# Optimization experiments

Measured on AMD Instinct MI355X. Metric: run time of the kernel, lower is better.

Reference implementation:

```python
import jax, jax.numpy as jnp
import numpy as np
from jax import lax

MSIZE = 64
NREG = 9
POOL_W = 256


def conv2d(x, w, b, stride):
    y = lax.conv_general_dilated(x, w, (stride, stride), ((1, 1), (1, 1)),
                                 dimension_numbers=('NCHW', 'OIHW', 'NCHW'))
    return y + b[None, :, None, None]


def resize_nearest(m, h, w):
    # nearest-neighbor resize of a 2D integer mask (matches cv2 INTER_NEAREST floor mapping)
    H, W = m.shape
    ri = (np.arange(h) * H) // h
    ci = (np.arange(w) * W) // w
    return m[ri][:, ci]


def adaptive_max_1d(x, out_size):
    # x: (c, N) -> (c, out_size), torch AdaptiveMaxPool semantics along last dim
    N = x.shape[1]
    j = np.arange(out_size)
    starts = (j * N) // out_size
    ends = -((-(j + 1) * N) // out_size)  # ceil((j+1)*N/out)
    maxlen = int((ends - starts).max())
    idx = starts[:, None] + np.arange(maxlen)[None, :]  # (out, maxlen)
    valid = idx < ends[:, None]
    idx = np.minimum(idx, N - 1)
    g = x[:, idx]  # (c, out, maxlen)
    g = jnp.where(valid[None, :, :], g, -jnp.inf)
    return g.max(axis=2)


def image_cnn(x, masks_np, w1, b1, w2, b2, w3, b3, fcw, fcb):
    f = jax.nn.relu(conv2d(x, w1, b1, 2))
    f = jax.nn.relu(conv2d(f, w2, b2, 2))
    f = conv2d(f, w3, b3, 2)
    _, c, h, w = f.shape
    ff = f.reshape(c, h * w)
    mats = {}
    for i in range(NREG):
        m = resize_nearest(masks_np[i, 0], h, w).reshape(-1)
        if int((m == 1).sum()) >= 10:
            idx = np.nonzero(m == 1)[0]
            pooled = adaptive_max_1d(ff[:, idx], POOL_W)  # (16, 256)
            mats[i] = fcw @ pooled.reshape(-1) + fcb      # (MSIZE*MSIZE,)
    return mats


def mul_forward(cF, sF, content, style, cmasks_np, smasks_np,
                compress_w, compress_b, unzip_w, unzip_b, sp, cp):
    sb, sc, sh, sw = sF.shape
    X = jnp.einsum('oc,bchw->bohw', compress_w, cF) + compress_b[None, :, None, None]
    cb, cc, ch, cw = X.shape
    X = X.reshape(cc, ch * cw)
    X = X - X.mean(axis=1, keepdims=True)
    sM = image_cnn(style, smasks_np, *sp)
    cM = image_cnn(content, cmasks_np, *cp)
    sFF = sF.reshape(sc, sh * sw)
    trans = X
    fmean = jnp.zeros((sc, ch * cw), dtype=cF.dtype)
    for i in range(NREG):
        cm = resize_nearest(cmasks_np[i, 0], ch, cw).reshape(-1)
        sm = resize_nearest(smasks_np[i, 0], sh, sw).reshape(-1)
        if int((cm == 1).sum()) >= 10 and int((sm == 1).sum()) >= 10 and i in sM and i in cM:
            fgc = np.nonzero(cm == 1)[0]
            fgs = np.nonzero(sm == 1)[0]
            sMean = sFF[:, fgs].mean(axis=1, keepdims=True)            # (sc, 1)
            T = sM[i].reshape(MSIZE, MSIZE) @ cM[i].reshape(MSIZE, MSIZE)
            trans = trans.at[:, fgc].set(T @ X[:, fgc])                 # gather-mm-scatter
            fmean = fmean.at[:, fgc].set(jnp.broadcast_to(sMean, (sc, fgc.size)))
    out = jnp.einsum('oc,bchw->bohw', unzip_w, trans.reshape(cb, cc, ch, cw)) \
          + unzip_b[None, :, None, None]
    return out + fmean.reshape(out.shape)


def setup_inputs():
    key = jax.random.key(0)
    ks = jax.random.split(key, 32)
    p = lambda k, s: jax.random.normal(k, s, dtype=jnp.float32) * 0.05
    inp = {}
    inp['cF'] = jax.random.normal(ks[0], (1, 256, 256, 256), dtype=jnp.float32)
    inp['sF'] = jax.random.normal(ks[1], (1, 256, 256, 256), dtype=jnp.float32)
    inp['content'] = jax.random.normal(ks[2], (1, 3, 1024, 1024), dtype=jnp.float32)
    inp['style'] = jax.random.normal(ks[3], (1, 3, 1024, 1024), dtype=jnp.float32)
    inp['cmasks'] = jax.random.randint(ks[4], (9, 1, 256, 256), 0, 2, dtype=jnp.int32)
    inp['smasks'] = jax.random.randint(ks[5], (9, 1, 256, 256), 0, 2, dtype=jnp.int32)
    inp['compress_w'] = p(ks[6], (MSIZE, 256))
    inp['compress_b'] = p(ks[7], (MSIZE,))
    inp['unzip_w'] = p(ks[8], (256, MSIZE))
    inp['unzip_b'] = p(ks[9], (256,))
    for pre, off in (('s', 10), ('c', 20)):
        inp[pre + '_w1'] = p(ks[off + 0], (64, 3, 3, 3))
        inp[pre + '_b1'] = p(ks[off + 1], (64,))
        inp[pre + '_w2'] = p(ks[off + 2], (32, 64, 3, 3))
        inp[pre + '_b2'] = p(ks[off + 3], (32,))
        inp[pre + '_w3'] = p(ks[off + 4], (16, 32, 3, 3))
        inp[pre + '_b3'] = p(ks[off + 5], (16,))
        inp[pre + '_fcw'] = p(ks[off + 6], (MSIZE * MSIZE, 16 * POOL_W))
        inp[pre + '_fcb'] = p(ks[off + 7], (MSIZE * MSIZE,))
    return inp


def reference(cF, sF, content, style, cmasks, smasks,
              compress_w, compress_b, unzip_w, unzip_b,
              s_w1, s_b1, s_w2, s_b2, s_w3, s_b3, s_fcw, s_fcb,
              c_w1, c_b1, c_w2, c_b2, c_w3, c_b3, c_fcw, c_fcb):
    cm_np = np.asarray(cmasks)
    sm_np = np.asarray(smasks)
    sp = (s_w1, s_b1, s_w2, s_b2, s_w3, s_b3, s_fcw, s_fcb)
    cp = (c_w1, c_b1, c_w2, c_b2, c_w3, c_b3, c_fcw, c_fcb)
    return mul_forward(cF, sF, content, style, cm_np, sm_np,
                       compress_w, compress_b, unzip_w, unzip_b, sp, cp)
```

## Files before the change

### kernel.cpp

```cpp
#include <hip/hip_runtime.h>
#include <math.h>

#define TPB 256
constexpr int YC_STRIDE = 68096;

constexpr size_t OFF_COUNTS   = 0x000000;
constexpr size_t OFF_ACTIVE   = 0x000100;
constexpr size_t OFF_LCNT     = 0x000140;
constexpr size_t OFF_RBASE    = 0x000180;
constexpr size_t OFF_MUSUM    = 0x000200;
constexpr size_t OFF_MU       = 0x000400;
constexpr size_t OFF_SSUM     = 0x000800;
constexpr size_t OFF_SMEAN    = 0x00A000;
constexpr size_t OFF_W1T      = 0x00D000;
constexpr size_t OFF_W3T      = 0x00F000;
constexpr size_t OFF_W2T      = 0x014000;
constexpr size_t OFF_CWT      = 0x028000;
constexpr size_t OFF_POOLED   = 0x040000;
constexpr size_t OFF_M        = 0x090000;
constexpr size_t OFF_P        = 0x0E0000;
constexpr size_t OFF_U        = 0x180000;
constexpr size_t OFF_V        = 0x228000;
constexpr size_t OFF_CBITS    = 0x230000;
constexpr size_t OFF_SBITS    = 0x270000;
constexpr size_t OFF_CBITS128 = 0x2B0000;
constexpr size_t OFF_SBITS128 = 0x2C0000;
constexpr size_t OFF_IDX      = 0x2D0000;
constexpr size_t OFF_BC       = 0x3F8000;
constexpr size_t OFF_BBASE    = 0x400000;
constexpr size_t OFF_RLIST    = 0x410000;
constexpr size_t OFF_INV      = 0x460000;
constexpr size_t OFF_XCT      = 0x700000;
constexpr size_t OFF_F1       = 0x1700000;
constexpr size_t OFF_F2       = 0x5700000;
constexpr size_t OFF_F3       = 0x5F00000;
constexpr size_t OFF_YC       = OFF_F1;

__global__ void init_k(int* p, int n) {
    for (int i = blockIdx.x * TPB + threadIdx.x; i < n; i += gridDim.x * TPB) p[i] = 0;
}

__global__ void bits_k(const int* __restrict__ cm, const int* __restrict__ sm,
                       int* __restrict__ cbits, int* __restrict__ sbits, int* __restrict__ counts) {
    int p = blockIdx.x * TPB + threadIdx.x;
    int cb = 0, sb = 0;
#pragma unroll
    for (int r = 0; r < 9; ++r) {
        cb |= (cm[r * 65536 + p] == 1) << r;
        sb |= (sm[r * 65536 + p] == 1) << r;
    }
    cbits[p] = cb; sbits[p] = sb;
    int lane = threadIdx.x & 63;
#pragma unroll
    for (int r = 0; r < 9; ++r) {
        unsigned long long b1 = __ballot((cb >> r) & 1);
        if (lane == 0) atomicAdd(&counts[0 + r], __popcll(b1));
        unsigned long long b2 = __ballot((sb >> r) & 1);
        if (lane == 0) atomicAdd(&counts[16 + r], __popcll(b2));
    }
}

__global__ void bits128_k(const int* __restrict__ cm, const int* __restrict__ sm,
                          int* __restrict__ cbits128, int* __restrict__ sbits128, int* __restrict__ counts) {
    int p = blockIdx.x * TPB + threadIdx.x;
    int y = p >> 7, x = p & 127;
    int src = (2 * y) * 256 + 2 * x;
    int cb = 0, sb = 0;
#pragma unroll
    for (int r = 0; r < 9; ++r) {
        cb |= (cm[r * 65536 + src] == 1) << r;
        sb |= (sm[r * 65536 + src] == 1) << r;
    }
    cbits128[p] = cb; sbits128[p] = sb;
    int lane = threadIdx.x & 63;
#pragma unroll
    for (int r = 0; r < 9; ++r) {
        unsigned long long b1 = __ballot((cb >> r) & 1);
        if (lane == 0) atomicAdd(&counts[32 + r], __popcll(b1));
        unsigned long long b2 = __ballot((sb >> r) & 1);
        if (lane == 0) atomicAdd(&counts[48 + r], __popcll(b2));
    }
}

__global__ void compact_k(const int* __restrict__ sbits128, const int* __restrict__ cbits128,
                          int* __restrict__ idxlist) {
    int r = blockIdx.x, side = blockIdx.y;
    const int* bits = side ? cbits128 : sbits128;
    int* outp = idxlist + (side * 9 + r) * 16384;
    __shared__ int wcnt[4];
    __shared__ int base_s;
    int t = threadIdx.x, w = t >> 6, lane = t & 63;
    if (t == 0) base_s = 0;
    __syncthreads();
    for (int chunk = 0; chunk < 64; ++chunk) {
        int pid = chunk * 256 + t;
        int flag = (bits[pid] >> r) & 1;
        unsigned long long m = __ballot(flag);
        if (lane == 0) wcnt[w] = __popcll(m);
        __syncthreads();
        int base = base_s;
        int woff = 0;
        for (int w2 = 0; w2 < w; ++w2) woff += wcnt[w2];
        if (flag) outp[base + woff + __popcll(m & ((1ull << lane) - 1ull))] = pid;
        __syncthreads();
        if (t == 0) base_s = base + wcnt[0] + wcnt[1] + wcnt[2] + wcnt[3];
    }
}

__global__ void wtr_k(const float* __restrict__ w, float* __restrict__ wT, int OC, int ICK) {
    int i = blockIdx.x * TPB + threadIdx.x;
    int n = OC * ICK;
    if (i < n) {
        int oc = i / ICK;
        int t = i - oc * ICK;
        wT[t * OC + oc] = w[i];
    }
}

__global__ void smean_k(const float* __restrict__ sF, const int* __restrict__ sbits,
                        float* __restrict__ ssump) {
    int c = blockIdx.x;
    int pg = blockIdx.y;
    int t = threadIdx.x;
    float acc[9];
#pragma unroll
    for (int r = 0; r < 9; ++r) acc[r] = 0.f;
    int p0 = pg * 16384;
    for (int p = p0 + t; p < p0 + 16384; p += TPB) {
        float v = sF[c * 65536 + p];
        int b = sbits[p];
#pragma unroll
        for (int r = 0; r < 9; ++r)
            if (b & (1 << r)) acc[r] += v;
    }
    __shared__ float red[9 * TPB];
#pragma unroll
    for (int r = 0; r < 9; ++r) red[r * TPB + t] = acc[r];
    __syncthreads();
    for (int off = TPB / 2; off > 0; off >>= 1) {
        if (t < off)
#pragma unroll
            for (int r = 0; r < 9; ++r) red[r * TPB + t] += red[r * TPB + t + off];
        __syncthreads();
    }
    if (t < 9) ssump[(pg * 9 + t) * 256 + c] = red[t * TPB];
}

__global__ void finalize_k(const int* __restrict__ counts, int* __restrict__ activemask,
                           const float* __restrict__ ssump, float* __restrict__ sMeanArr) {
    __shared__ int am;
    if (threadIdx.x == 0) am = 0;
    __syncthreads();
    if (threadIdx.x < 9) {
        int r = threadIdx.x;
        if (counts[0 + r] >= 10 && counts[16 + r] >= 10 && counts[32 + r] >= 10 && counts[48 + r] >= 10)
            atomicOr(&am, 1 << r);
    }
    __syncthreads();
    if (threadIdx.x == 0) *activemask = am;
    for (int e = threadIdx.x; e < 2560; e += TPB) {
        int r = e >> 8, c = e & 255;
        float v = 0.f;
        if (r < 9 && ((am >> r) & 1)) {
            float s = ssump[(0 * 9 + r) * 256 + c] + ssump[(1 * 9 + r) * 256 + c]
                    + ssump[(2 * 9 + r) * 256 + c] + ssump[(3 * 9 + r) * 256 + c];
            v = s / (float)counts[16 + r];
        }
        sMeanArr[e] = v;
    }
}

__global__ void hist_k(const int* __restrict__ cbits, const int* __restrict__ activemask,
                       int* __restrict__ rmap, int* __restrict__ bc) {
    int b = blockIdx.x, t = threadIdx.x;
    int p = b * 256 + t;
    int am = *activemask;
    int bits = cbits[p] & am;
    int r = bits ? (31 - __clz(bits)) : 9;
    rmap[p] = r;
    __shared__ int wc[4][10];
    int w = t >> 6, lane = t & 63;
#pragma unroll
    for (int rr = 0; rr < 10; ++rr) {
        unsigned long long m = __ballot(r == rr);
        if (lane == rr) wc[w][rr] = __popcll(m);
    }
    __syncthreads();
    if (t < 10) bc[b * 10 + t] = wc[0][t] + wc[1][t] + wc[2][t] + wc[3][t];
}

__global__ void scan_k(const int* __restrict__ bc, int* __restrict__ bbase,
                       int* __restrict__ lcnt, int* __restrict__ rbase) {
    __shared__ int tot[10], Bs[16];
    int t = threadIdx.x;
    if (t < 10) {
        int s = 0;
        for (int b = 0; b < 256; ++b) s += bc[b * 10 + t];
        tot[t] = s;
    }
    __syncthreads();
    if (t == 0) {
        int run = 0;
        for (int r = 0; r < 10; ++r) { Bs[r] = run; run += (tot[r] + 255) & ~255; }
    }
    __syncthreads();
    if (t < 10) {
        lcnt[t] = tot[t];
        rbase[t] = Bs[t];
        int run = Bs[t];
        for (int b = 0; b < 256; ++b) { bbase[b * 10 + t] = run; run += bc[b * 10 + t]; }
    }
}

__global__ void rank_k(const int* __restrict__ rmap, const int* __restrict__ bbase,
                       int* __restrict__ inv, int* __restrict__ rlist) {
    int b = blockIdx.x, t = threadIdx.x;
    int p = b * 256 + t;
    int r = rmap[p];
    __shared__ int wc[4][10];
    int w = t >> 6, lane = t & 63;
    int prefix = 0;
#pragma unroll
    for (int rr = 0; rr < 10; ++rr) {
        unsigned long long m = __ballot(r == rr);
        if (rr == r) prefix = __popcll(m & ((1ull << lane) - 1ull));
        if (lane == rr) wc[w][rr] = __popcll(m);
    }
    __syncthreads();
    int woff = 0;
    for (int w2 = 0; w2 < w; ++w2) woff += wc[w2][r];
    int g = bbase[b * 10 + r] + woff + prefix;
    inv[p] = g;
    rlist[g] = p;
}

__global__ void conv1_k(const float* __restrict__ in, const float* __restrict__ wT,
                        const float* __restrict__ b, float* __restrict__ out) {
    int idx = blockIdx.x * TPB + threadIdx.x;
    int og = blockIdx.y;
    int ox = idx & 511, oy = idx >> 9;
    float acc[32];
#pragma unroll
    for (int oc = 0; oc < 32; ++oc) acc[oc] = b[og * 32 + oc];
    for (int ic = 0; ic < 3; ++ic)
#pragma unroll
        for (int ky = 0; ky < 3; ++ky) {
            int iy = 2 * oy - 1 + ky;
            if ((unsigned)iy < 1024u)
#pragma unroll
                for (int kx = 0; kx < 3; ++kx) {
                    int ix = 2 * ox - 1 + kx;
                    if ((unsigned)ix < 1024u) {
                        float v = in[ic * 1048576 + iy * 1024 + ix];
                        const float4* wp = (const float4*)(wT + (ic * 9 + ky * 3 + kx) * 64 + og * 32);
#pragma unroll
                        for (int q = 0; q < 8; ++q) {
                            float4 w4 = wp[q];
                            acc[q * 4 + 0] = fmaf(w4.x, v, acc[q * 4 + 0]);
                            acc[q * 4 + 1] = fmaf(w4.y, v, acc[q * 4 + 1]);
                            acc[q * 4 + 2] = fmaf(w4.z, v, acc[q * 4 + 2]);
                            acc[q * 4 + 3] = fmaf(w4.w, v, acc[q * 4 + 3]);
                        }
                    }
                }
        }
#pragma unroll
    for (int oc = 0; oc < 32; ++oc) out[(og * 32 + oc) * 262144 + idx] = fmaxf(acc[oc], 0.f);
}

__global__ void f2init_k(const float* __restrict__ b, float* __restrict__ F2) {
    int idx = blockIdx.x * TPB + threadIdx.x;
#pragma unroll
    for (int oc = 0; oc < 32; ++oc) F2[oc * 65536 + idx] = b[oc];
}

__global__ void conv2p_k(const float* __restrict__ in, const float* __restrict__ wT,
                         float* __restrict__ F2) {
    int idx = blockIdx.x * TPB + threadIdx.x;
    int icg = blockIdx.y;
    int ox = idx & 255, oy = idx >> 8;
    float acc[32];
#pragma unroll
    for (int oc = 0; oc < 32; ++oc) acc[oc] = 0.f;
    for (int ic = icg * 16; ic < icg * 16 + 16; ++ic) {
        const float* base = in + ic * 262144;
#pragma unroll
        for (int ky = 0; ky < 3; ++ky) {
            int iy = 2 * oy - 1 + ky;
            if ((unsigned)iy < 512u)
#pragma unroll
                for (int kx = 0; kx < 3; ++kx) {
                    int ix = 2 * ox - 1 + kx;
                    if ((unsigned)ix < 512u) {
                        float v = base[iy * 512 + ix];
                        const float4* wp = (const float4*)(wT + (ic * 9 + ky * 3 + kx) * 32);
#pragma unroll
                        for (int q = 0; q < 8; ++q) {
                            float4 w4 = wp[q];
                            acc[q * 4 + 0] = fmaf(w4.x, v, acc[q * 4 + 0]);
                            acc[q * 4 + 1] = fmaf(w4.y, v, acc[q * 4 + 1]);
                            acc[q * 4 + 2] = fmaf(w4.z, v, acc[q * 4 + 2]);
                            acc[q * 4 + 3] = fmaf(w4.w, v, acc[q * 4 + 3]);
                        }
                    }
                }
        }
    }
#pragma unroll
    for (int oc = 0; oc < 32; ++oc) atomicAdd(&F2[oc * 65536 + idx], acc[oc]);
}

__global__ void relu2_k(float* __restrict__ F2) {
    int i = blockIdx.x * TPB + threadIdx.x;
    float4* p = (float4*)F2;
    float4 v = p[i];
    v.x = fmaxf(v.x, 0.f); v.y = fmaxf(v.y, 0.f);
    v.z = fmaxf(v.z, 0.f); v.w = fmaxf(v.w, 0.f);
    p[i] = v;
}

__global__ void f3init_k(const float* __restrict__ b, float* __restrict__ F3) {
    int idx = blockIdx.x * TPB + threadIdx.x;
#pragma unroll
    for (int oc = 0; oc < 16; ++oc) F3[oc * 16384 + idx] = b[oc];
}

__global__ void conv3p_k(const float* __restrict__ in, const float* __restrict__ wT,
                         float* __restrict__ F3) {
    int idx = blockIdx.x * TPB + threadIdx.x;
    int icg = blockIdx.y;
    int ox = idx & 127, oy = idx >> 7;
    float acc[16];
#pragma unroll
    for (int oc = 0; oc < 16; ++oc) acc[oc] = 0.f;
    for (int ic = icg * 8; ic < icg * 8 + 8; ++ic) {
        const float* base = in + ic * 65536;
#pragma unroll
        for (int ky = 0; ky < 3; ++ky) {
            int iy = 2 * oy - 1 + ky;
            if ((unsigned)iy < 256u)
#pragma unroll
                for (int kx = 0; kx < 3; ++kx) {
                    int ix = 2 * ox - 1 + kx;
                    if ((unsigned)ix < 256u) {
                        float v = base[iy * 256 + ix];
                        const float4* wp = (const float4*)(wT + (ic * 9 + ky * 3 + kx) * 16);
#pragma unroll
                        for (int q = 0; q < 4; ++q) {
                            float4 w4 = wp[q];
                            acc[q * 4 + 0] = fmaf(w4.x, v, acc[q * 4 + 0]);
                            acc[q * 4 + 1] = fmaf(w4.y, v, acc[q * 4 + 1]);
                            acc[q * 4 + 2] = fmaf(w4.z, v, acc[q * 4 + 2]);
                            acc[q * 4 + 3] = fmaf(w4.w, v, acc[q * 4 + 3]);
                        }
                    }
                }
        }
    }
#pragma unroll
    for (int oc = 0; oc < 16; ++oc) atomicAdd(&F3[oc * 16384 + idx], acc[oc]);
}

__global__ void pool_k(const float* __restrict__ f3, const int* __restrict__ idxbase,
                       const int* __restrict__ cnt, float* __restrict__ pooled) {
    int r = blockIdx.x >> 4;
    int c = blockIdx.x & 15;
    int j = threadIdx.x;
    int n = cnt[r];
    float m = 0.f;
    if (n >= 1) {
        int start = (j * n) >> 8;
        int end = ((j + 1) * n + 255) >> 8;
        const int* il = idxbase + r * 16384;
        m = -__builtin_inff();
        for (int t = start; t < end; ++t) m = fmaxf(m, f3[c * 16384 + il[t]]);
    }
    pooled[(r * 16 + c) * 256 + j] = m;
}

__global__ void fc_k(const float* __restrict__ fcw_s, const float* __restrict__ fcb_s,
                     const float* __restrict__ fcw_c, const float* __restrict__ fcb_c,
                     const float* __restrict__ pooled, float* __restrict__ Mout) {
    int row = blockIdx.x;
    int side = blockIdx.y;
    const float* fcw = side ? fcw_c : fcw_s;
    const float* fcb = side ? fcb_c : fcb_s;
    const float* P = pooled + side * 9 * 4096;
    int t = threadIdx.x;
    float acc[9];
#pragma unroll
    for (int r = 0; r < 9; ++r) acc[r] = 0.f;
    for (int k = t; k < 4096; k += TPB) {
        float w = fcw[row * 4096 + k];
#pragma unroll
        for (int r = 0; r < 9; ++r) acc[r] = fmaf(w, P[r * 4096 + k], acc[r]);
    }
    __shared__ float red[9 * TPB];
#pragma unroll
    for (int r = 0; r < 9; ++r) red[r * TPB + t] = acc[r];
    __syncthreads();
    for (int off = TPB / 2; off > 0; off >>= 1) {
        if (t < off)
#pragma unroll
            for (int r = 0; r < 9; ++r) red[r * TPB + t] += red[r * TPB + t + off];
        __syncthreads();
    }
    if (t < 9) Mout[(side * 9 + t) * 4096 + row] = red[t * TPB] + fcb[row];
}

__global__ void xgemm_k(const float* __restrict__ cF, const float* __restrict__ cwT,
                        float* __restrict__ XcT) {
    int p = blockIdx.x * TPB + threadIdx.x;
    int m0 = blockIdx.y * 16;
    float acc[16];
#pragma unroll
    for (int m = 0; m < 16; ++m) acc[m] = 0.f;
    for (int k0 = 0; k0 < 256; k0 += 4) {
        float xv[4];
#pragma unroll
        for (int i = 0; i < 4; ++i) xv[i] = cF[(k0 + i) * 65536 + p];
#pragma unroll
        for (int i = 0; i < 4; ++i) {
            const float4* wp = (const float4*)(cwT + (k0 + i) * 64 + m0);
#pragma unroll
            for (int q = 0; q < 4; ++q) {
                float4 w4 = wp[q];
                acc[q * 4 + 0] = fmaf(w4.x, xv[i], acc[q * 4 + 0]);
                acc[q * 4 + 1] = fmaf(w4.y, xv[i], acc[q * 4 + 1]);
                acc[q * 4 + 2] = fmaf(w4.z, xv[i], acc[q * 4 + 2]);
                acc[q * 4 + 3] = fmaf(w4.w, xv[i], acc[q * 4 + 3]);
            }
        }
    }
    float4* op = (float4*)(XcT + p * 64 + m0);
#pragma unroll
    for (int q = 0; q < 4; ++q)
        op[q] = make_float4(acc[q * 4 + 0], acc[q * 4 + 1], acc[q * 4 + 2], acc[q * 4 + 3]);
}

__global__ void muacc_k(const float* __restrict__ XcT, float* __restrict__ musum) {
    int t = threadIdx.x;
    int m = t & 63, sub = t >> 6;
    int p0 = blockIdx.x * 256;
    float a = 0.f;
    for (int i = 0; i < 64; ++i) a += XcT[(p0 + sub + i * 4) * 64 + m];
    __shared__ float red[TPB];
    red[t] = a;
    __syncthreads();
    if (t < 64) atomicAdd(&musum[t], red[t] + red[t + 64] + red[t + 128] + red[t + 192]);
}

__global__ void mufin_k(const float* __restrict__ musum, float* __restrict__ mu) {
    int t = threadIdx.x;
    if (t < 64) mu[t] = musum[t] * (1.f / 65536.f);
}

__global__ void uprep1_k(const float* __restrict__ uw, const float* __restrict__ M,
                         float* __restrict__ P) {
    int idx = blockIdx.x * TPB + threadIdx.x;
    int r = idx / 16384;
    int rem = idx & 16383;
    int c = rem >> 6, k = rem & 63;
    float a = 0.f;
#pragma unroll 8
    for (int i = 0; i < 64; ++i) a = fmaf(uw[c * 64 + i], M[r * 4096 + i * 64 + k], a);
    P[idx] = a;
}

__global__ void uprep2_k(const float* __restrict__ uw, const float* __restrict__ M,
                         const float* __restrict__ P, float* __restrict__ U) {
    int idx = blockIdx.x * TPB + threadIdx.x;
    int r = idx / 16384;
    int rem = idx & 16383;
    int c = rem >> 6, j = rem & 63;
    if (r == 9) { U[idx] = uw[c * 64 + j]; return; }
    float a = 0.f;
#pragma unroll 8
    for (int k = 0; k < 64; ++k) a = fmaf(P[r * 16384 + c * 64 + k], M[(9 + r) * 4096 + k * 64 + j], a);
    U[idx] = a;
}

__global__ void uprep3_k(const float* __restrict__ U, const float* __restrict__ mu,
                         const float* __restrict__ uzb, const float* __restrict__ sMeanArr,
                         float* __restrict__ V) {
    int r = blockIdx.x;
    int c = threadIdx.x;
    float a = uzb[c] + sMeanArr[r * 256 + c];
#pragma unroll 8
    for (int j = 0; j < 64; ++j) a -= U[r * 16384 + c * 64 + j] * mu[j];
    V[r * 256 + c] = a;
}

__global__ void ygemm_k(const float* __restrict__ XcT, const float* __restrict__ U,
                        const float* __restrict__ V, const int* __restrict__ lcnt,
                        const int* __restrict__ rbase, const int* __restrict__ rlist,
                        float* __restrict__ Yc) {
    int r = blockIdx.x >> 8;
    int c = blockIdx.x & 255;
    int ocg = blockIdx.y;
    int n = lcnt[r];
    int start = c * 256;
    if (start >= n) return;
    int i = start + threadIdx.x;
    bool valid = i < n;
    int gi = rbase[r] + (valid ? i : n - 1);
    int pix = rlist[gi];
    float4 xv[16];
    const float4* xp = (const float4*)(XcT + (size_t)pix * 64);
#pragma unroll
    for (int q = 0; q < 16; ++q) xv[q] = xp[q];
    const float* Ur = U + r * 16384 + ocg * 4096;
    const float* Vr = V + r * 256 + ocg * 64;
#pragma unroll 4
    for (int oc = 0; oc < 64; ++oc) {
        float a = Vr[oc];
        const float4* up = (const float4*)(Ur + oc * 64);
#pragma unroll
        for (int q = 0; q < 16; ++q) {
            float4 u4 = up[q];
            a = fmaf(u4.x, xv[q].x, a);
            a = fmaf(u4.y, xv[q].y, a);
            a = fmaf(u4.z, xv[q].z, a);
            a = fmaf(u4.w, xv[q].w, a);
        }
        if (valid) Yc[(size_t)(ocg * 64 + oc) * YC_STRIDE + gi] = a;
    }
}

__global__ void merge_k(const float* __restrict__ Yc, const int* __restrict__ inv,
                        float* __restrict__ out) {
    int p = blockIdx.x * TPB + threadIdx.x;
    int oc0 = blockIdx.y * 4;
    int gi = inv[p];
#pragma unroll
    for (int j = 0; j < 4; ++j)
        out[(size_t)(oc0 + j) * 65536 + p] = Yc[(size_t)(oc0 + j) * YC_STRIDE + gi];
}

extern "C" void kernel_launch(void* const* d_in, const int* in_sizes, int n_in,
                              void* d_out, int out_size, void* d_ws, size_t ws_size,
                              hipStream_t stream) {
    const float* cF         = (const float*)d_in[0];
    const float* sF         = (const float*)d_in[1];
    const float* content    = (const float*)d_in[2];
    const float* style      = (const float*)d_in[3];
    const int*   cmasks     = (const int*)d_in[4];
    const int*   smasks     = (const int*)d_in[5];
    const float* compress_w = (const float*)d_in[6];
    const float* unzip_w    = (const float*)d_in[8];
    const float* unzip_b    = (const float*)d_in[9];
    const float* s_w1 = (const float*)d_in[10]; const float* s_b1 = (const float*)d_in[11];
    const float* s_w2 = (const float*)d_in[12]; const float* s_b2 = (const float*)d_in[13];
    const float* s_w3 = (const float*)d_in[14]; const float* s_b3 = (const float*)d_in[15];
    const float* s_fcw = (const float*)d_in[16]; const float* s_fcb = (const float*)d_in[17];
    const float* c_w1 = (const float*)d_in[18]; const float* c_b1 = (const float*)d_in[19];
    const float* c_w2 = (const float*)d_in[20]; const float* c_b2 = (const float*)d_in[21];
    const float* c_w3 = (const float*)d_in[22]; const float* c_b3 = (const float*)d_in[23];
    const float* c_fcw = (const float*)d_in[24]; const float* c_fcb = (const float*)d_in[25];
    float* out = (float*)d_out;
    char* ws = (char*)d_ws;
#define WF(o) ((float*)(ws + (o)))
#define WI(o) ((int*)(ws + (o)))

    init_k<<<1, TPB, 0, stream>>>(WI(0), 256);
    bits_k<<<256, TPB, 0, stream>>>(cmasks, smasks, WI(OFF_CBITS), WI(OFF_SBITS), WI(OFF_COUNTS));
    bits128_k<<<64, TPB, 0, stream>>>(cmasks, smasks, WI(OFF_CBITS128), WI(OFF_SBITS128), WI(OFF_COUNTS));
    compact_k<<<dim3(9, 2), TPB, 0, stream>>>(WI(OFF_SBITS128), WI(OFF_CBITS128), WI(OFF_IDX));
    smean_k<<<dim3(256, 4), TPB, 0, stream>>>(sF, WI(OFF_SBITS), WF(OFF_SSUM));
    finalize_k<<<1, TPB, 0, stream>>>(WI(OFF_COUNTS), WI(OFF_ACTIVE), WF(OFF_SSUM), WF(OFF_SMEAN));

    hist_k<<<256, TPB, 0, stream>>>(WI(OFF_CBITS), WI(OFF_ACTIVE), WI(OFF_INV) , WI(OFF_BC));
    scan_k<<<1, TPB, 0, stream>>>(WI(OFF_BC), WI(OFF_BBASE), WI(OFF_LCNT), WI(OFF_RBASE));
    rank_k<<<256, TPB, 0, stream>>>(WI(OFF_INV) , WI(OFF_BBASE), WI(OFF_INV), WI(OFF_RLIST));

    wtr_k<<<64, TPB, 0, stream>>>(compress_w, WF(OFF_CWT), 64, 256);
    xgemm_k<<<dim3(256, 4), TPB, 0, stream>>>(cF, WF(OFF_CWT), WF(OFF_XCT));
    muacc_k<<<256, TPB, 0, stream>>>(WF(OFF_XCT), WF(OFF_MUSUM));
    mufin_k<<<1, 64, 0, stream>>>(WF(OFF_MUSUM), WF(OFF_MU));

    wtr_k<<<7, TPB, 0, stream>>>(s_w1, WF(OFF_W1T), 64, 27);
    wtr_k<<<72, TPB, 0, stream>>>(s_w2, WF(OFF_W2T), 32, 576);
    wtr_k<<<18, TPB, 0, stream>>>(s_w3, WF(OFF_W3T), 16, 288);
    conv1_k<<<dim3(1024, 2), TPB, 0, stream>>>(style, WF(OFF_W1T), s_b1, WF(OFF_F1));
    f2init_k<<<256, TPB, 0, stream>>>(s_b2, WF(OFF_F2));
    conv2p_k<<<dim3(256, 4), TPB, 0, stream>>>(WF(OFF_F1), WF(OFF_W2T), WF(OFF_F2));
    relu2_k<<<2048, TPB, 0, stream>>>(WF(OFF_F2));
    f3init_k<<<64, TPB, 0, stream>>>(s_b3, WF(OFF_F3));
    conv3p_k<<<dim3(64, 4), TPB, 0, stream>>>(WF(OFF_F2), WF(OFF_W3T), WF(OFF_F3));
    pool_k<<<144, TPB, 0, stream>>>(WF(OFF_F3), WI(OFF_IDX), WI(OFF_COUNTS) + 48, WF(OFF_POOLED));

    wtr_k<<<7, TPB, 0, stream>>>(c_w1, WF(OFF_W1T), 64, 27);
    wtr_k<<<72, TPB, 0, stream>>>(c_w2, WF(OFF_W2T), 32, 576);
    wtr_k<<<18, TPB, 0, stream>>>(c_w3, WF(OFF_W3T), 16, 288);
    conv1_k<<<dim3(1024, 2), TPB, 0, stream>>>(content, WF(OFF_W1T), c_b1, WF(OFF_F1));
    f2init_k<<<256, TPB, 0, stream>>>(c_b2, WF(OFF_F2));
    conv2p_k<<<dim3(256, 4), TPB, 0, stream>>>(WF(OFF_F1), WF(OFF_W2T), WF(OFF_F2));
    relu2_k<<<2048, TPB, 0, stream>>>(WF(OFF_F2));
    f3init_k<<<64, TPB, 0, stream>>>(c_b3, WF(OFF_F3));
    conv3p_k<<<dim3(64, 4), TPB, 0, stream>>>(WF(OFF_F2), WF(OFF_W3T), WF(OFF_F3));
    pool_k<<<144, TPB, 0, stream>>>(WF(OFF_F3), WI(OFF_IDX) + 9 * 16384, WI(OFF_COUNTS) + 32,
                                    WF(OFF_POOLED) + 9 * 4096);

    fc_k<<<dim3(4096, 2), TPB, 0, stream>>>(s_fcw, s_fcb, c_fcw, c_fcb, WF(OFF_POOLED), WF(OFF_M));

    uprep1_k<<<576, TPB, 0, stream>>>(unzip_w, WF(OFF_M), WF(OFF_P));
    uprep2_k<<<640, TPB, 0, stream>>>(unzip_w, WF(OFF_M), WF(OFF_P), WF(OFF_U));
    uprep3_k<<<10, TPB, 0, stream>>>(WF(OFF_U), WF(OFF_MU), unzip_b, WF(OFF_SMEAN), WF(OFF_V));

    ygemm_k<<<dim3(2560, 4), TPB, 0, stream>>>(WF(OFF_XCT), WF(OFF_U), WF(OFF_V),
                                               WI(OFF_LCNT), WI(OFF_RBASE), WI(OFF_RLIST), WF(OFF_YC));
    merge_k<<<dim3(256, 64), TPB, 0, stream>>>(WF(OFF_YC), WI(OFF_INV), out);
}
```

Measured before the change: 1.099 ms.

## Stage conv1 and conv2 input rows in LDS with double-buffered channel loads

conv1 and conv2 now load each needed input row segment into shared memory with coalesced float4 reads. Each thread then reads its stride-2 taps from LDS instead of doing strided, bounds-checked global loads. conv2 double-buffers the tile across input channels so the next channel's global load overlaps compute on the current one. Launch bounds are added to cap registers, and block-to-pixel mapping is reorganized to one output row per block.

Result: no change. 1.118 ms (+1.7%).

```diff
diff --git a/kernel.cpp b/kernel.cpp
--- a/kernel.cpp
+++ b/kernel.cpp
@@ -234,36 +234,56 @@
     rlist[g] = p;
 }
 
-__global__ void conv1_k(const float* __restrict__ in, const float* __restrict__ wT,
-                        const float* __restrict__ b, float* __restrict__ out) {
-    int idx = blockIdx.x * TPB + threadIdx.x;
+__global__ __launch_bounds__(256, 4) void conv1_k(const float* __restrict__ in,
+                                                  const float* __restrict__ wT,
+                                                  const float* __restrict__ b,
+                                                  float* __restrict__ out) {
+    int oy = blockIdx.x >> 1;
+    int X0 = (blockIdx.x & 1) << 8;
     int og = blockIdx.y;
-    int ox = idx & 511, oy = idx >> 9;
+    int t = threadIdx.x;
+    __shared__ float tile[3][3][520];
+    for (int u = t; u < 1152; u += 256) {
+        int ic = u / 384;
+        int rem = u - ic * 384;
+        int row = rem >> 7, q = rem & 127;
+        int iy = 2 * oy - 1 + row;
+        float4 v = make_float4(0.f, 0.f, 0.f, 0.f);
+        if ((unsigned)iy < 1024u)
+            v = *(const float4*)(in + ic * 1048576 + iy * 1024 + 2 * X0 + 4 * q);
+        float* dst = &tile[ic][row][1 + 4 * q];
+        dst[0] = v.x; dst[1] = v.y; dst[2] = v.z; dst[3] = v.w;
+    }
+    if (t < 9) {
+        int ic = t / 3, row = t % 3;
+        int iy = 2 * oy - 1 + row;
+        int ix = 2 * X0 - 1;
+        float v = 0.f;
+        if ((unsigned)iy < 1024u && ix >= 0) v = in[ic * 1048576 + iy * 1024 + ix];
+        tile[ic][row][0] = v;
+    }
+    __syncthreads();
     float acc[32];
 #pragma unroll
     for (int oc = 0; oc < 32; ++oc) acc[oc] = b[og * 32 + oc];
+#pragma unroll
     for (int ic = 0; ic < 3; ++ic)
 #pragma unroll
-        for (int ky = 0; ky < 3; ++ky) {
-            int iy = 2 * oy - 1 + ky;
-            if ((unsigned)iy < 1024u)
-#pragma unroll
-                for (int kx = 0; kx < 3; ++kx) {
-                    int ix = 2 * ox - 1 + kx;
-                    if ((unsigned)ix < 1024u) {
-                        float v = in[ic * 1048576 + iy * 1024 + ix];
-                        const float4* wp = (const float4*)(wT + (ic * 9 + ky * 3 + kx) * 64 + og * 32);
-#pragma unroll
-                        for (int q = 0; q < 8; ++q) {
-                            float4 w4 = wp[q];
-                            acc[q * 4 + 0] = fmaf(w4.x, v, acc[q * 4 + 0]);
-                            acc[q * 4 + 1] = fmaf(w4.y, v, acc[q * 4 + 1]);
-                            acc[q * 4 + 2] = fmaf(w4.z, v, acc[q * 4 + 2]);
-                            acc[q * 4 + 3] = fmaf(w4.w, v, acc[q * 4 + 3]);
-                        }
-                    }
+        for (int ky = 0; ky < 3; ++ky)
+#pragma unroll
+            for (int kx = 0; kx < 3; ++kx) {
+                float v = tile[ic][ky][2 * t + kx];
+                const float4* wp = (const float4*)(wT + (ic * 9 + ky * 3 + kx) * 64 + og * 32);
+#pragma unroll
+                for (int q = 0; q < 8; ++q) {
+                    float4 w4 = wp[q];
+                    acc[q * 4 + 0] = fmaf(w4.x, v, acc[q * 4 + 0]);
+                    acc[q * 4 + 1] = fmaf(w4.y, v, acc[q * 4 + 1]);
+                    acc[q * 4 + 2] = fmaf(w4.z, v, acc[q * 4 + 2]);
+                    acc[q * 4 + 3] = fmaf(w4.w, v, acc[q * 4 + 3]);
                 }
-        }
+            }
+    int idx = oy * 512 + X0 + t;
 #pragma unroll
     for (int oc = 0; oc < 32; ++oc) out[(og * 32 + oc) * 262144 + idx] = fmaxf(acc[oc], 0.f);
 }
@@ -274,38 +294,76 @@
     for (int oc = 0; oc < 32; ++oc) F2[oc * 65536 + idx] = b[oc];
 }
 
-__global__ void conv2p_k(const float* __restrict__ in, const float* __restrict__ wT,
-                         float* __restrict__ F2) {
-    int idx = blockIdx.x * TPB + threadIdx.x;
+__device__ __forceinline__ void c2_load(const float* __restrict__ base, int oy, int t,
+                                        float4& r0, float4& r1) {
+    int row0 = t >> 7, q0 = t & 127;
+    int iy0 = 2 * oy - 1 + row0;
+    r0 = make_float4(0.f, 0.f, 0.f, 0.f);
+    if ((unsigned)iy0 < 512u) r0 = *(const float4*)(base + iy0 * 512 + 4 * q0);
+    r1 = make_float4(0.f, 0.f, 0.f, 0.f);
+    if (t < 128) {
+        int iy1 = 2 * oy + 1;
+        r1 = *(const float4*)(base + iy1 * 512 + 4 * t);
+    }
+}
+
+__device__ __forceinline__ void c2_store(float (*tile)[520], int t, float4 r0, float4 r1) {
+    int row0 = t >> 7, q0 = t & 127;
+    float* d0 = &tile[row0][1 + 4 * q0];
+    d0[0] = r0.x; d0[1] = r0.y; d0[2] = r0.z; d0[3] = r0.w;
+    if (t < 128) {
+        float* d1 = &tile[2][1 + 4 * t];
+        d1[0] = r1.x; d1[1] = r1.y; d1[2] = r1.z; d1[3] = r1.w;
+    }
+}
+
+__device__ __forceinline__ void c2_compute(const float* __restrict__ wT, int ic,
+                                           const float (*tile)[520], int t, float* acc) {
+#pragma unroll
+    for (int ky = 0; ky < 3; ++ky)
+#pragma unroll
+        for (int kx = 0; kx < 3; ++kx) {
+            float v = tile[ky][2 * t + kx];
+            const float4* wp = (const float4*)(wT + (ic * 9 + ky * 3 + kx) * 32);
+#pragma unroll
+            for (int q = 0; q < 8; ++q) {
+                float4 w4 = wp[q];
+                acc[q * 4 + 0] = fmaf(w4.x, v, acc[q * 4 + 0]);
+                acc[q * 4 + 1] = fmaf(w4.y, v, acc[q * 4 + 1]);
+                acc[q * 4 + 2] = fmaf(w4.z, v, acc[q * 4 + 2]);
+                acc[q * 4 + 3] = fmaf(w4.w, v, acc[q * 4 + 3]);
+            }
+        }
+}
+
+__global__ __launch_bounds__(256, 4) void conv2p_k(const float* __restrict__ in,
+                                                   const float* __restrict__ wT,
+                                                   float* __restrict__ F2) {
+    int oy = blockIdx.x;
     int icg = blockIdx.y;
-    int ox = idx & 255, oy = idx >> 8;
+    int t = threadIdx.x;
+    __shared__ float tile[2][3][520];
+    if (t < 6) tile[t / 3][t % 3][0] = 0.f;
     float acc[32];
 #pragma unroll
     for (int oc = 0; oc < 32; ++oc) acc[oc] = 0.f;
-    for (int ic = icg * 16; ic < icg * 16 + 16; ++ic) {
-        const float* base = in + ic * 262144;
-#pragma unroll
-        for (int ky = 0; ky < 3; ++ky) {
-            int iy = 2 * oy - 1 + ky;
-            if ((unsigned)iy < 512u)
-#pragma unroll
-                for (int kx = 0; kx < 3; ++kx) {
-                    int ix = 2 * ox - 1 + kx;
-                    if ((unsigned)ix < 512u) {
-                        float v = base[iy * 512 + ix];
-                        const float4* wp = (const float4*)(wT + (ic * 9 + ky * 3 + kx) * 32);
-#pragma unroll
-                        for (int q = 0; q < 8; ++q) {
-                            float4 w4 = wp[q];
-                            acc[q * 4 + 0] = fmaf(w4.x, v, acc[q * 4 + 0]);
-                            acc[q * 4 + 1] = fmaf(w4.y, v, acc[q * 4 + 1]);
-                            acc[q * 4 + 2] = fmaf(w4.z, v, acc[q * 4 + 2]);
-                            acc[q * 4 + 3] = fmaf(w4.w, v, acc[q * 4 + 3]);
-                        }
-                    }
-                }
-        }
-    }
+    int ic0 = icg * 16;
+    float4 r0, r1;
+    c2_load(in + ic0 * 262144, oy, t, r0, r1);
+    c2_store(tile[0], t, r0, r1);
+    __syncthreads();
+#pragma unroll 1
+    for (int i = 0; i < 16; i += 2) {
+        c2_load(in + (ic0 + i + 1) * 262144, oy, t, r0, r1);
+        c2_compute(wT, ic0 + i, tile[0], t, acc);
+        c2_store(tile[1], t, r0, r1);
+        __syncthreads();
+        if (i + 2 < 16) c2_load(in + (ic0 + i + 2) * 262144, oy, t, r0, r1);
+        c2_compute(wT, ic0 + i + 1, tile[1], t, acc);
+        if (i + 2 < 16) c2_store(tile[0], t, r0, r1);
+        __syncthreads();
+    }
+    int idx = oy * 256 + t;
 #pragma unroll
     for (int oc = 0; oc < 32; ++oc) atomicAdd(&F2[oc * 65536 + idx], acc[oc]);
 }
```
